# Performance work log

Measured on AMD Instinct MI355X. Metric: run time of the kernel, lower is better.

The kernel has to match this reference:

```python
import jax, jax.numpy as jnp
import numpy as np

BN_EPS = 1e-5
K = 3  # number of nearest neighbors for interpolation


def setup_inputs() -> dict:
    key = jax.random.key(0)
    ks = jax.random.split(key, 16)
    B, N1, N2 = 8, 8192, 2048
    C2, C1, H = 256, 128, 256  # in_channels, skip_channels, out_channels
    total_in = C2 + C1
    inp = {
        "xyz1": jax.random.normal(ks[0], (B, 3, N1), dtype=jnp.float32),
        "xyz2": jax.random.normal(ks[1], (B, 3, N2), dtype=jnp.float32),
        "features1": jax.random.normal(ks[2], (B, C1, N1), dtype=jnp.float32),
        "features2": jax.random.normal(ks[3], (B, C2, N2), dtype=jnp.float32),
        # SharedMLP([total_in, H, H]): two 1x1 Conv1d + BatchNorm1d (eval mode) + ReLU
        "w1": jax.random.normal(ks[4], (H, total_in), dtype=jnp.float32) * 0.05,
        "b1": jax.random.normal(ks[5], (H,), dtype=jnp.float32) * 0.01,
        "g1": 1.0 + 0.1 * jax.random.normal(ks[6], (H,), dtype=jnp.float32),
        "be1": 0.1 * jax.random.normal(ks[7], (H,), dtype=jnp.float32),
        "m1": 0.1 * jax.random.normal(ks[8], (H,), dtype=jnp.float32),
        "v1": 0.5 + jax.random.uniform(ks[9], (H,), dtype=jnp.float32),
        "w2": jax.random.normal(ks[10], (H, H), dtype=jnp.float32) * 0.05,
        "b2": jax.random.normal(ks[11], (H,), dtype=jnp.float32) * 0.01,
        "g2": 1.0 + 0.1 * jax.random.normal(ks[12], (H,), dtype=jnp.float32),
        "be2": 0.1 * jax.random.normal(ks[13], (H,), dtype=jnp.float32),
        "m2": 0.1 * jax.random.normal(ks[14], (H,), dtype=jnp.float32),
        "v2": 0.5 + jax.random.uniform(ks[15], (H,), dtype=jnp.float32),
    }
    return inp


def _conv_bn_relu(x, w, b, g, be, m, v):
    # x: [B, Cin, N], w: [Cout, Cin] (1x1 conv), BN in eval mode
    y = jnp.einsum("oc,bcn->bon", w, x) + b[None, :, None]
    y = (y - m[None, :, None]) * (g / jnp.sqrt(v + BN_EPS))[None, :, None] + be[None, :, None]
    return jax.nn.relu(y)


def reference(xyz1, xyz2, features1, features2,
              w1, b1, g1, be1, m1, v1,
              w2, b2, g2, be2, m2, v2):
    # --- squared pairwise distances [B, N1, N2] ---
    x1 = jnp.transpose(xyz1, (0, 2, 1))  # [B, N1, 3]
    x2 = jnp.transpose(xyz2, (0, 2, 1))  # [B, N2, 3]
    sq = (jnp.sum(x1 * x1, axis=-1, keepdims=True)
          + jnp.sum(x2 * x2, axis=-1)[:, None, :]
          - 2.0 * jnp.einsum("bnd,bmd->bnm", x1, x2))
    # --- k=3 nearest neighbors (smallest sq distances) ---
    neg_d, idx = jax.lax.top_k(-sq, K)          # [B, N1, K]
    dist = jnp.maximum(-neg_d, 1e-10)
    weight = 1.0 / dist
    weight = weight / jnp.sum(weight, axis=-1, keepdims=True)  # [B, N1, K]
    # --- gather neighbor features and inverse-distance interpolate ---
    feat2_t = jnp.transpose(features2, (0, 2, 1))              # [B, N2, C2]
    neighbor = jax.vmap(lambda f, i: f[i])(feat2_t, idx)       # [B, N1, K, C2]
    interp = jnp.einsum("bnkc,bnk->bnc", neighbor, weight)     # [B, N1, C2]
    interp = jnp.transpose(interp, (0, 2, 1))                  # [B, C2, N1]
    # --- concat skip features and shared MLP ---
    x = jnp.concatenate([interp, features1], axis=1)           # [B, C2+C1, N1]
    x = _conv_bn_relu(x, w1, b1, g1, be1, m1, v1)
    x = _conv_bn_relu(x, w2, b2, g2, be2, m2, v2)
    return x
```

## Files before the change

kernel.cpp:

```cpp
#include <hip/hip_runtime.h>
#include <hip/hip_bf16.h>

typedef unsigned short u16;
typedef __attribute__((ext_vector_type(4))) float f32x4;
typedef __attribute__((ext_vector_type(8))) short short8;

#define BN_EPS 1e-5f

__device__ __forceinline__ u16 f2b(float x) {
  union { float f; unsigned int u; } v; v.f = x;
  unsigned int r = (v.u + 0x7FFFu + ((v.u >> 16) & 1u)) >> 16;
  return (u16)r;
}
__device__ __forceinline__ float b2f(u16 u) {
  union { unsigned int u; float f; } v; v.u = ((unsigned int)u) << 16;
  return v.f;
}
__device__ __forceinline__ float asf(unsigned u) {
  union { unsigned u; float f; } v; v.u = u; return v.f;
}

__global__ void prep_transpose_kernel(
    const float* __restrict__ f2, u16* __restrict__ f2t,
    const float* __restrict__ w1, const float* __restrict__ b1,
    const float* __restrict__ g1, const float* __restrict__ be1,
    const float* __restrict__ m1, const float* __restrict__ v1,
    const float* __restrict__ w2, const float* __restrict__ b2,
    const float* __restrict__ g2, const float* __restrict__ be2,
    const float* __restrict__ m2, const float* __restrict__ v2,
    u16* __restrict__ w1b, u16* __restrict__ w2b,
    float* __restrict__ al1, float* __restrict__ bt1,
    float* __restrict__ al2, float* __restrict__ bt2) {
  __shared__ float tile[32][33];
  int t = threadIdx.x;
  int blk = blockIdx.x;
  if (blk < 4096) {
    int tx = t & 31, ty = t >> 5;
    int b = (blk >> 9) & 7;
    int n2t = (blk & 63) * 32, ct = ((blk >> 6) & 7) * 32;
#pragma unroll
    for (int i = 0; i < 4; ++i) {
      int c = ct + ty + i * 8;
      tile[ty + i * 8][tx] = f2[((size_t)b * 256 + c) * 2048 + n2t + tx];
    }
    __syncthreads();
#pragma unroll
    for (int i = 0; i < 4; ++i) {
      int n2 = n2t + ty + i * 8;
      f2t[((size_t)b * 2048 + n2) * 256 + ct + tx] = f2b(tile[tx][ty + i * 8]);
    }
  } else if (blk < 4480) {
    int id = (blk - 4096) * 256 + t;
    unsigned o = (unsigned)id / 384u;
    unsigned c = (unsigned)id % 384u;
    w1b[(c >> 5) * 8192 + o * 32 + (c & 31)] = f2b(w1[id]);
  } else if (blk < 4736) {
    int j = (blk - 4480) * 256 + t;
    unsigned o = (unsigned)j >> 8;
    unsigned c = (unsigned)j & 255u;
    w2b[(c >> 5) * 8192 + o * 32 + (c & 31)] = f2b(w2[j]);
  } else if (blk == 4736) {
    float a = g1[t] / sqrtf(v1[t] + BN_EPS);
    al1[t] = a;
    bt1[t] = (b1[t] - m1[t]) * a + be1[t];
  } else {
    float a = g2[t] / sqrtf(v2[t] + BN_EPS);
    al2[t] = a;
    bt2[t] = (b2[t] - m2[t]) * a + be2[t];
  }
}

__global__ __launch_bounds__(256) void knn_interp_kernel(
    const float* __restrict__ xyz1, const float* __restrict__ xyz2,
    const float* __restrict__ f1, const u16* __restrict__ f2t,
    u16* __restrict__ xb) {
  union Lds {
    struct { float4 pts[2048]; float md[256 * 3]; u16 mi[256 * 3]; } a;
    float f1t[128 * 65];
  };
  __shared__ Lds lds;
  __shared__ float wts[64 * 3];
  __shared__ int idxs[64 * 3];

  int t = threadIdx.x;
  int b = blockIdx.x >> 7;
  int n1_0 = (blockIdx.x & 127) * 64;
  int panel = blockIdx.x;

  const float* x2 = xyz2 + b * 3 * 2048;
  for (int j = t; j < 2048; j += 256) {
    float cx = x2[j], cy = x2[2048 + j], cz = x2[4096 + j];
    float nsq = (cx * cx + cy * cy) + cz * cz;
    lds.a.pts[j] = make_float4(cx, cy, cz, nsq);
  }
  __syncthreads();

  const float* x1 = xyz1 + b * 3 * 8192;

  {
    int p = t & 63, s = t >> 6;
    int n1 = n1_0 + p;
    float bx = x1[n1], by = x1[8192 + n1], bz = x1[16384 + n1];
    float nx = -2.f * bx, ny = -2.f * by, nz = -2.f * bz;
    float d0 = 3.4e38f, d1 = 3.4e38f, d2 = 3.4e38f;
    int i0 = 0, i1 = 0, i2 = 0;
    int jb = s * 512;

#define KNN_UPD(cv, jv)                                                      \
    {                                                                        \
      float sq = fmaf(nx, (cv).x, fmaf(ny, (cv).y, fmaf(nz, (cv).z, (cv).w))); \
      if (__any(sq < d2)) {                                                  \
        bool c0 = sq < d0, c1 = sq < d1, c2 = sq < d2;                       \
        i2 = c1 ? i1 : (c2 ? (jv) : i2);                                     \
        i1 = c0 ? i0 : (c1 ? (jv) : i1);                                     \
        i0 = c0 ? (jv) : i0;                                                 \
        d2 = __builtin_amdgcn_fmed3f(sq, d1, d2);                            \
        d1 = __builtin_amdgcn_fmed3f(sq, d0, d1);                            \
        d0 = fminf(sq, d0);                                                  \
      }                                                                      \
    }

    for (int jj = 0; jj < 512; jj += 4) {
      float4 ca = lds.a.pts[jb + jj + 0];
      float4 cb = lds.a.pts[jb + jj + 1];
      float4 cc = lds.a.pts[jb + jj + 2];
      float4 cd = lds.a.pts[jb + jj + 3];
      KNN_UPD(ca, jb + jj + 0);
      KNN_UPD(cb, jb + jj + 1);
      KNN_UPD(cc, jb + jj + 2);
      KNN_UPD(cd, jb + jj + 3);
    }
#undef KNN_UPD
    lds.a.md[t * 3 + 0] = d0; lds.a.md[t * 3 + 1] = d1; lds.a.md[t * 3 + 2] = d2;
    lds.a.mi[t * 3 + 0] = (u16)i0; lds.a.mi[t * 3 + 1] = (u16)i1; lds.a.mi[t * 3 + 2] = (u16)i2;
  }
  __syncthreads();
  if (t < 64) {
    float d0 = 3.4e38f, d1 = 3.4e38f, d2 = 3.4e38f;
    int i0 = 0, i1 = 0, i2 = 0;
#pragma unroll
    for (int s = 0; s < 4; ++s) {
#pragma unroll
      for (int k = 0; k < 3; ++k) {
        float d = lds.a.md[(s * 64 + t) * 3 + k];
        int i = (int)lds.a.mi[(s * 64 + t) * 3 + k];
        bool c0 = d < d0, c1 = d < d1, c2 = d < d2;
        i2 = c1 ? i1 : (c2 ? i : i2);
        i1 = c0 ? i0 : (c1 ? i : i1);
        i0 = c0 ? i : i0;
        d2 = c1 ? d1 : (c2 ? d : d2);
        d1 = c0 ? d0 : (c1 ? d : d1);
        d0 = c0 ? d : d0;
      }
    }
    int n1 = n1_0 + t;
    float bx = x1[n1], by = x1[8192 + n1], bz = x1[16384 + n1];
    float nn = (bx * bx + by * by) + bz * bz;
    float e0 = fmaxf(d0 + nn, 1e-10f), e1 = fmaxf(d1 + nn, 1e-10f), e2 = fmaxf(d2 + nn, 1e-10f);
    float w0 = 1.0f / e0, w1 = 1.0f / e1, w2 = 1.0f / e2;
    float sm = (w0 + w1) + w2;
    wts[t * 3 + 0] = w0 / sm; wts[t * 3 + 1] = w1 / sm; wts[t * 3 + 2] = w2 / sm;
    idxs[t * 3 + 0] = i0 * 256; idxs[t * 3 + 1] = i1 * 256; idxs[t * 3 + 2] = i2 * 256;
  }
  __syncthreads();

  {
    const u16* f2tb = f2t + (size_t)b * 2048 * 256;
    int tc = t & 63;
    int qg = t >> 6;
    int ce = (4 * tc) & 31;
    size_t xbase = (size_t)panel * 24576 + (size_t)(tc >> 3) * 2048 + ce;
#pragma unroll 4
    for (int p2 = 0; p2 < 16; ++p2) {
      int p = p2 * 4 + qg;
      int j0 = idxs[p * 3 + 0], j1 = idxs[p * 3 + 1], j2 = idxs[p * 3 + 2];
      float w0 = wts[p * 3 + 0], w1 = wts[p * 3 + 1], w2 = wts[p * 3 + 2];
      uint2 a0 = *(const uint2*)&f2tb[j0 + 4 * tc];
      uint2 a1 = *(const uint2*)&f2tb[j1 + 4 * tc];
      uint2 a2 = *(const uint2*)&f2tb[j2 + 4 * tc];
      float v0 = (w0 * asf(a0.x << 16) + w1 * asf(a1.x << 16)) + w2 * asf(a2.x << 16);
      float v1 = (w0 * asf(a0.x & 0xffff0000u) + w1 * asf(a1.x & 0xffff0000u))
                 + w2 * asf(a2.x & 0xffff0000u);
      float v2 = (w0 * asf(a0.y << 16) + w1 * asf(a1.y << 16)) + w2 * asf(a2.y << 16);
      float v3 = (w0 * asf(a0.y & 0xffff0000u) + w1 * asf(a1.y & 0xffff0000u))
                 + w2 * asf(a2.y & 0xffff0000u);
      uint2 pk;
      pk.x = (unsigned)f2b(v0) | ((unsigned)f2b(v1) << 16);
      pk.y = (unsigned)f2b(v2) | ((unsigned)f2b(v3) << 16);
      *(uint2*)&xb[xbase + (size_t)p * 32] = pk;
    }
  }
  __syncthreads();

  {
    const float* f1b = f1 + (size_t)b * 128 * 8192 + n1_0;
    for (int it = 0; it < 32; ++it) {
      int c = it * 4 + (t >> 6);
      int n = t & 63;
      lds.f1t[c * 65 + n] = f1b[(size_t)c * 8192 + n];
    }
    __syncthreads();
    for (int it = 0; it < 32; ++it) {
      int v = it * 256 + t;
      int c = v & 127, p = v >> 7;
      float val = lds.f1t[c * 65 + p];
      xb[(size_t)panel * 24576 + (size_t)(8 + (c >> 5)) * 2048 + p * 32 + (c & 31)] = f2b(val);
    }
  }
}

__global__ __launch_bounds__(256) void gemm_fused_kernel(
    const u16* __restrict__ xin, const u16* __restrict__ w1b,
    const u16* __restrict__ w2b,
    const float* __restrict__ al1, const float* __restrict__ bt1,
    const float* __restrict__ al2, const float* __restrict__ bt2,
    float* __restrict__ fout) {
  __shared__ u16 y1t[8 * 64 * 40];
  int t = threadIdx.x;
  int panel = blockIdx.x;
  int w = t >> 6, lane = t & 63, l15 = lane & 15, quad = lane >> 4;

  f32x4 acc[4][4];
#pragma unroll
  for (int m = 0; m < 4; ++m)
#pragma unroll
    for (int n = 0; n < 4; ++n)
      acc[m][n] = (f32x4){0.f, 0.f, 0.f, 0.f};

  {
    const u16* aw = w1b + (size_t)(w * 64 + l15) * 32 + quad * 8;
    const u16* bx = xin + (size_t)panel * 24576 + (size_t)l15 * 32 + quad * 8;
    short8 af[2][4], bf[2][4];
#pragma unroll
    for (int m = 0; m < 4; ++m)
      af[0][m] = *(const short8*)(aw + m * 512);
#pragma unroll
    for (int n = 0; n < 4; ++n)
      bf[0][n] = *(const short8*)(bx + n * 512);
#pragma unroll
    for (int kt = 0; kt < 12; ++kt) {
      int cur = kt & 1, nxt = cur ^ 1;
      if (kt < 11) {
#pragma unroll
        for (int m = 0; m < 4; ++m)
          af[nxt][m] = *(const short8*)(aw + (kt + 1) * 8192 + m * 512);
#pragma unroll
        for (int n = 0; n < 4; ++n)
          bf[nxt][n] = *(const short8*)(bx + (kt + 1) * 2048 + n * 512);
      }
#pragma unroll
      for (int m = 0; m < 4; ++m)
#pragma unroll
        for (int n = 0; n < 4; ++n)
          acc[m][n] = __builtin_amdgcn_mfma_f32_16x16x32_bf16(af[cur][m], bf[cur][n], acc[m][n], 0, 0, 0);
    }
  }

  {
    float al[4][4], bt[4][4];
#pragma unroll
    for (int m = 0; m < 4; ++m)
#pragma unroll
      for (int r = 0; r < 4; ++r) {
        int o = w * 64 + m * 16 + quad * 4 + r;
        al[m][r] = al1[o];
        bt[m][r] = bt1[o];
      }
#pragma unroll
    for (int m = 0; m < 4; ++m) {
      int kt2 = w * 2 + (m >> 1);
      int osub = (m & 1) * 16 + quad * 4;
#pragma unroll
      for (int n = 0; n < 4; ++n) {
        int col = n * 16 + l15;
        ushort4 pk;
        pk.x = f2b(fmaxf(fmaf(al[m][0], acc[m][n][0], bt[m][0]), 0.f));
        pk.y = f2b(fmaxf(fmaf(al[m][1], acc[m][n][1], bt[m][1]), 0.f));
        pk.z = f2b(fmaxf(fmaf(al[m][2], acc[m][n][2], bt[m][2]), 0.f));
        pk.w = f2b(fmaxf(fmaf(al[m][3], acc[m][n][3], bt[m][3]), 0.f));
        *(ushort4*)&y1t[(kt2 * 64 + col) * 40 + osub] = pk;
      }
    }
  }
  __syncthreads();

#pragma unroll
  for (int m = 0; m < 4; ++m)
#pragma unroll
    for (int n = 0; n < 4; ++n)
      acc[m][n] = (f32x4){0.f, 0.f, 0.f, 0.f};
  {
    const u16* aw = w2b + (size_t)(w * 64 + l15) * 32 + quad * 8;
    short8 af[2][4];
#pragma unroll
    for (int m = 0; m < 4; ++m)
      af[0][m] = *(const short8*)(aw + m * 512);
#pragma unroll
    for (int kt = 0; kt < 8; ++kt) {
      int cur = kt & 1, nxt = cur ^ 1;
      if (kt < 7) {
#pragma unroll
        for (int m = 0; m < 4; ++m)
          af[nxt][m] = *(const short8*)(aw + (kt + 1) * 8192 + m * 512);
      }
      short8 bf[4];
#pragma unroll
      for (int n = 0; n < 4; ++n)
        bf[n] = *(const short8*)&y1t[(kt * 64 + n * 16 + l15) * 40 + quad * 8];
#pragma unroll
      for (int m = 0; m < 4; ++m)
#pragma unroll
        for (int n = 0; n < 4; ++n)
          acc[m][n] = __builtin_amdgcn_mfma_f32_16x16x32_bf16(af[cur][m], bf[n], acc[m][n], 0, 0, 0);
    }
  }

  {
    float al[4][4], bt[4][4];
#pragma unroll
    for (int m = 0; m < 4; ++m)
#pragma unroll
      for (int r = 0; r < 4; ++r) {
        int o = w * 64 + m * 16 + quad * 4 + r;
        al[m][r] = al2[o];
        bt[m][r] = bt2[o];
      }
    int bb = panel >> 7;
    int n1base = (panel & 127) * 64;
#pragma unroll
    for (int m = 0; m < 4; ++m)
#pragma unroll
      for (int n = 0; n < 4; ++n) {
        int col = n * 16 + l15;
#pragma unroll
        for (int r = 0; r < 4; ++r) {
          int o = w * 64 + m * 16 + quad * 4 + r;
          float vv = fmaxf(fmaf(al[m][r], acc[m][n][r], bt[m][r]), 0.f);
          fout[(size_t)(bb * 256 + o) * 8192 + n1base + col] = vv;
        }
      }
  }
}

extern "C" void kernel_launch(void* const* d_in, const int* in_sizes, int n_in,
                              void* d_out, int out_size, void* d_ws, size_t ws_size,
                              hipStream_t stream) {
  const float* xyz1 = (const float*)d_in[0];
  const float* xyz2 = (const float*)d_in[1];
  const float* f1   = (const float*)d_in[2];
  const float* f2   = (const float*)d_in[3];
  const float* w1   = (const float*)d_in[4];
  const float* b1   = (const float*)d_in[5];
  const float* g1   = (const float*)d_in[6];
  const float* be1  = (const float*)d_in[7];
  const float* m1   = (const float*)d_in[8];
  const float* v1   = (const float*)d_in[9];
  const float* w2   = (const float*)d_in[10];
  const float* b2   = (const float*)d_in[11];
  const float* g2   = (const float*)d_in[12];
  const float* be2  = (const float*)d_in[13];
  const float* m2   = (const float*)d_in[14];
  const float* v2   = (const float*)d_in[15];

  char* ws = (char*)d_ws;
  u16* xb   = (u16*)(ws);
  u16* f2t  = (u16*)(ws + 50331648);
  u16* w1b  = (u16*)(ws + 83886080);
  u16* w2b  = (u16*)(ws + 84082688);
  float* al1 = (float*)(ws + 84213760);
  float* bt1 = (float*)(ws + 84214784);
  float* al2 = (float*)(ws + 84215808);
  float* bt2 = (float*)(ws + 84216832);
  float* out = (float*)d_out;

  prep_transpose_kernel<<<4738, 256, 0, stream>>>(
      f2, f2t, w1, b1, g1, be1, m1, v1, w2, b2, g2, be2, m2, v2,
      w1b, w2b, al1, bt1, al2, bt2);
  knn_interp_kernel<<<1024, 256, 0, stream>>>(xyz1, xyz2, f1, f2t, xb);
  gemm_fused_kernel<<<1024, 256, 0, stream>>>(xb, w1b, w2b, al1, bt1, al2, bt2, out);
}
```

Before: 217.4 us.

## Precompute xyz2 float4 table in prep kernel and read KNN candidates from global

Moves the per-block packing of xyz2 into (x,y,z,|x|^2) float4 entries out of the KNN kernel and into extra blocks of the prep kernel, which write a global table. The KNN loop then reads candidate points straight from global memory (uniform addresses, so effectively scalar or broadcast loads through cache) instead of staging 32KB in LDS. This removes the LDS fill, a barrier and most of the LDS footprint, which can raise occupancy. The cost is that the inner loop now depends on global or cache load latency instead of LDS reads.

```diff
diff --git a/kernel.cpp b/kernel.cpp
--- a/kernel.cpp
+++ b/kernel.cpp
@@ -28,9 +28,11 @@
     const float* __restrict__ w2, const float* __restrict__ b2,
     const float* __restrict__ g2, const float* __restrict__ be2,
     const float* __restrict__ m2, const float* __restrict__ v2,
+    const float* __restrict__ xyz2,
     u16* __restrict__ w1b, u16* __restrict__ w2b,
     float* __restrict__ al1, float* __restrict__ bt1,
-    float* __restrict__ al2, float* __restrict__ bt2) {
+    float* __restrict__ al2, float* __restrict__ bt2,
+    float4* __restrict__ c4i) {
   __shared__ float tile[32][33];
   int t = threadIdx.x;
   int blk = blockIdx.x;
@@ -63,19 +65,27 @@
     float a = g1[t] / sqrtf(v1[t] + BN_EPS);
     al1[t] = a;
     bt1[t] = (b1[t] - m1[t]) * a + be1[t];
-  } else {
+  } else if (blk == 4737) {
     float a = g2[t] / sqrtf(v2[t] + BN_EPS);
     al2[t] = a;
     bt2[t] = (b2[t] - m2[t]) * a + be2[t];
+  } else {
+    int idx = (blk - 4738) * 256 + t;
+    int bb = idx >> 11, j = idx & 2047;
+    float cx = xyz2[bb * 6144 + j];
+    float cy = xyz2[bb * 6144 + 2048 + j];
+    float cz = xyz2[bb * 6144 + 4096 + j];
+    float nsq = (cx * cx + cy * cy) + cz * cz;
+    c4i[bb * 2048 + j] = make_float4(cx, cy, cz, nsq);
   }
 }
 
 __global__ __launch_bounds__(256) void knn_interp_kernel(
-    const float* __restrict__ xyz1, const float* __restrict__ xyz2,
+    const float* __restrict__ xyz1, const float4* __restrict__ c4i,
     const float* __restrict__ f1, const u16* __restrict__ f2t,
     u16* __restrict__ xb) {
   union Lds {
-    struct { float4 pts[2048]; float md[256 * 3]; u16 mi[256 * 3]; } a;
+    struct { float md[256 * 3]; u16 mi[256 * 3]; } a;
     float f1t[128 * 65];
   };
   __shared__ Lds lds;
@@ -87,14 +97,6 @@
   int n1_0 = (blockIdx.x & 127) * 64;
   int panel = blockIdx.x;
 
-  const float* x2 = xyz2 + b * 3 * 2048;
-  for (int j = t; j < 2048; j += 256) {
-    float cx = x2[j], cy = x2[2048 + j], cz = x2[4096 + j];
-    float nsq = (cx * cx + cy * cy) + cz * cz;
-    lds.a.pts[j] = make_float4(cx, cy, cz, nsq);
-  }
-  __syncthreads();
-
   const float* x1 = xyz1 + b * 3 * 8192;
 
   {
@@ -102,6 +104,7 @@
     int n1 = n1_0 + p;
     float bx = x1[n1], by = x1[8192 + n1], bz = x1[16384 + n1];
     float nx = -2.f * bx, ny = -2.f * by, nz = -2.f * bz;
+    const float4* cp = c4i + b * 2048;
     float d0 = 3.4e38f, d1 = 3.4e38f, d2 = 3.4e38f;
     int i0 = 0, i1 = 0, i2 = 0;
     int jb = s * 512;
@@ -121,10 +124,10 @@
     }
 
     for (int jj = 0; jj < 512; jj += 4) {
-      float4 ca = lds.a.pts[jb + jj + 0];
-      float4 cb = lds.a.pts[jb + jj + 1];
-      float4 cc = lds.a.pts[jb + jj + 2];
-      float4 cd = lds.a.pts[jb + jj + 3];
+      float4 ca = cp[jb + jj + 0];
+      float4 cb = cp[jb + jj + 1];
+      float4 cc = cp[jb + jj + 2];
+      float4 cd = cp[jb + jj + 3];
       KNN_UPD(ca, jb + jj + 0);
       KNN_UPD(cb, jb + jj + 1);
       KNN_UPD(cc, jb + jj + 2);
@@ -363,19 +366,20 @@
   const float* v2   = (const float*)d_in[15];
 
   char* ws = (char*)d_ws;
-  u16* xb   = (u16*)(ws);
-  u16* f2t  = (u16*)(ws + 50331648);
-  u16* w1b  = (u16*)(ws + 83886080);
-  u16* w2b  = (u16*)(ws + 84082688);
+  u16* xb    = (u16*)(ws);
+  u16* f2t   = (u16*)(ws + 50331648);
+  float4* c4i = (float4*)(ws + 58720256);
+  u16* w1b   = (u16*)(ws + 83886080);
+  u16* w2b   = (u16*)(ws + 84082688);
   float* al1 = (float*)(ws + 84213760);
   float* bt1 = (float*)(ws + 84214784);
   float* al2 = (float*)(ws + 84215808);
   float* bt2 = (float*)(ws + 84216832);
   float* out = (float*)d_out;
 
-  prep_transpose_kernel<<<4738, 256, 0, stream>>>(
+  prep_transpose_kernel<<<4802, 256, 0, stream>>>(
       f2, f2t, w1, b1, g1, be1, m1, v1, w2, b2, g2, be2, m2, v2,
-      w1b, w2b, al1, bt1, al2, bt2);
-  knn_interp_kernel<<<1024, 256, 0, stream>>>(xyz1, xyz2, f1, f2t, xb);
+      xyz2, w1b, w2b, al1, bt1, al2, bt2, c4i);
+  knn_interp_kernel<<<1024, 256, 0, stream>>>(xyz1, c4i, f1, f2t, xb);
   gemm_fused_kernel<<<1024, 256, 0, stream>>>(xb, w1b, w2b, al1, bt1, al2, bt2, out);
 }
```

Result: slower. 240.8 us (+10.8%).

## Fuse kNN interpolation and MLP GEMMs into one kernel via LDS staging

Applied to the files above, without the earlier changes.

Merges the kNN/interpolation kernel and the two-layer MLP GEMM kernel into a single kernel per 64-point panel. The concatenated bf16 input tile is built directly in shared memory (Bt) rather than written to a global workspace and read back. This removes a global round trip of the activation buffer and one kernel launch. In exchange, shared-memory use per block grows, which may reduce occupancy, and the kNN phase and the MFMA phase can no longer overlap across separate kernels.

```diff
diff --git a/kernel.cpp b/kernel.cpp
--- a/kernel.cpp
+++ b/kernel.cpp
@@ -70,28 +70,33 @@
   }
 }
 
-__global__ __launch_bounds__(256) void knn_interp_kernel(
+__global__ __launch_bounds__(256) void fp_fused_kernel(
     const float* __restrict__ xyz1, const float* __restrict__ xyz2,
     const float* __restrict__ f1, const u16* __restrict__ f2t,
-    u16* __restrict__ xb) {
-  union Lds {
+    const u16* __restrict__ w1b, const u16* __restrict__ w2b,
+    const float* __restrict__ al1, const float* __restrict__ bt1,
+    const float* __restrict__ al2, const float* __restrict__ bt2,
+    float* __restrict__ fout) {
+  union U {
     struct { float4 pts[2048]; float md[256 * 3]; u16 mi[256 * 3]; } a;
     float f1t[128 * 65];
+    u16 y1t[8 * 64 * 40];
   };
-  __shared__ Lds lds;
+  __shared__ U u;
+  __shared__ u16 Bt[12 * 64 * 40];
   __shared__ float wts[64 * 3];
   __shared__ int idxs[64 * 3];
 
   int t = threadIdx.x;
-  int b = blockIdx.x >> 7;
-  int n1_0 = (blockIdx.x & 127) * 64;
   int panel = blockIdx.x;
+  int b = panel >> 7;
+  int n1_0 = (panel & 127) * 64;
 
   const float* x2 = xyz2 + b * 3 * 2048;
   for (int j = t; j < 2048; j += 256) {
     float cx = x2[j], cy = x2[2048 + j], cz = x2[4096 + j];
     float nsq = (cx * cx + cy * cy) + cz * cz;
-    lds.a.pts[j] = make_float4(cx, cy, cz, nsq);
+    u.a.pts[j] = make_float4(cx, cy, cz, nsq);
   }
   __syncthreads();
 
@@ -121,18 +126,18 @@
     }
 
     for (int jj = 0; jj < 512; jj += 4) {
-      float4 ca = lds.a.pts[jb + jj + 0];
-      float4 cb = lds.a.pts[jb + jj + 1];
-      float4 cc = lds.a.pts[jb + jj + 2];
-      float4 cd = lds.a.pts[jb + jj + 3];
+      float4 ca = u.a.pts[jb + jj + 0];
+      float4 cb = u.a.pts[jb + jj + 1];
+      float4 cc = u.a.pts[jb + jj + 2];
+      float4 cd = u.a.pts[jb + jj + 3];
       KNN_UPD(ca, jb + jj + 0);
       KNN_UPD(cb, jb + jj + 1);
       KNN_UPD(cc, jb + jj + 2);
       KNN_UPD(cd, jb + jj + 3);
     }
 #undef KNN_UPD
-    lds.a.md[t * 3 + 0] = d0; lds.a.md[t * 3 + 1] = d1; lds.a.md[t * 3 + 2] = d2;
-    lds.a.mi[t * 3 + 0] = (u16)i0; lds.a.mi[t * 3 + 1] = (u16)i1; lds.a.mi[t * 3 + 2] = (u16)i2;
+    u.a.md[t * 3 + 0] = d0; u.a.md[t * 3 + 1] = d1; u.a.md[t * 3 + 2] = d2;
+    u.a.mi[t * 3 + 0] = (u16)i0; u.a.mi[t * 3 + 1] = (u16)i1; u.a.mi[t * 3 + 2] = (u16)i2;
   }
   __syncthreads();
   if (t < 64) {
@@ -142,8 +147,8 @@
     for (int s = 0; s < 4; ++s) {
 #pragma unroll
       for (int k = 0; k < 3; ++k) {
-        float d = lds.a.md[(s * 64 + t) * 3 + k];
-        int i = (int)lds.a.mi[(s * 64 + t) * 3 + k];
+        float d = u.a.md[(s * 64 + t) * 3 + k];
+        int i = (int)u.a.mi[(s * 64 + t) * 3 + k];
         bool c0 = d < d0, c1 = d < d1, c2 = d < d2;
         i2 = c1 ? i1 : (c2 ? i : i2);
         i1 = c0 ? i0 : (c1 ? i : i1);
@@ -169,7 +174,7 @@
     int tc = t & 63;
     int qg = t >> 6;
     int ce = (4 * tc) & 31;
-    size_t xbase = (size_t)panel * 24576 + (size_t)(tc >> 3) * 2048 + ce;
+    int bbase = (tc >> 3) * 2560 + ce;
 #pragma unroll 4
     for (int p2 = 0; p2 < 16; ++p2) {
       int p = p2 * 4 + qg;
@@ -187,37 +192,27 @@
       uint2 pk;
       pk.x = (unsigned)f2b(v0) | ((unsigned)f2b(v1) << 16);
       pk.y = (unsigned)f2b(v2) | ((unsigned)f2b(v3) << 16);
-      *(uint2*)&xb[xbase + (size_t)p * 32] = pk;
-    }
-  }
-  __syncthreads();
+      *(uint2*)&Bt[bbase + p * 40] = pk;
+    }
+  }
 
   {
     const float* f1b = f1 + (size_t)b * 128 * 8192 + n1_0;
     for (int it = 0; it < 32; ++it) {
       int c = it * 4 + (t >> 6);
       int n = t & 63;
-      lds.f1t[c * 65 + n] = f1b[(size_t)c * 8192 + n];
+      u.f1t[c * 65 + n] = f1b[(size_t)c * 8192 + n];
     }
     __syncthreads();
     for (int it = 0; it < 32; ++it) {
       int v = it * 256 + t;
       int c = v & 127, p = v >> 7;
-      float val = lds.f1t[c * 65 + p];
-      xb[(size_t)panel * 24576 + (size_t)(8 + (c >> 5)) * 2048 + p * 32 + (c & 31)] = f2b(val);
-    }
-  }
-}
-
-__global__ __launch_bounds__(256) void gemm_fused_kernel(
-    const u16* __restrict__ xin, const u16* __restrict__ w1b,
-    const u16* __restrict__ w2b,
-    const float* __restrict__ al1, const float* __restrict__ bt1,
-    const float* __restrict__ al2, const float* __restrict__ bt2,
-    float* __restrict__ fout) {
-  __shared__ u16 y1t[8 * 64 * 40];
-  int t = threadIdx.x;
-  int panel = blockIdx.x;
+      float val = u.f1t[c * 65 + p];
+      Bt[(8 + (c >> 5)) * 2560 + p * 40 + (c & 31)] = f2b(val);
+    }
+  }
+  __syncthreads();
+
   int w = t >> 6, lane = t & 63, l15 = lane & 15, quad = lane >> 4;
 
   f32x4 acc[4][4];
@@ -229,14 +224,10 @@
 
   {
     const u16* aw = w1b + (size_t)(w * 64 + l15) * 32 + quad * 8;
-    const u16* bx = xin + (size_t)panel * 24576 + (size_t)l15 * 32 + quad * 8;
-    short8 af[2][4], bf[2][4];
+    short8 af[2][4];
 #pragma unroll
     for (int m = 0; m < 4; ++m)
       af[0][m] = *(const short8*)(aw + m * 512);
-#pragma unroll
-    for (int n = 0; n < 4; ++n)
-      bf[0][n] = *(const short8*)(bx + n * 512);
 #pragma unroll
     for (int kt = 0; kt < 12; ++kt) {
       int cur = kt & 1, nxt = cur ^ 1;
@@ -244,15 +235,16 @@
 #pragma unroll
         for (int m = 0; m < 4; ++m)
           af[nxt][m] = *(const short8*)(aw + (kt + 1) * 8192 + m * 512);
+      }
+      short8 bf[4];
+#pragma unroll
+      for (int n = 0; n < 4; ++n)
+        bf[n] = *(const short8*)&Bt[kt * 2560 + (n * 16 + l15) * 40 + quad * 8];
+#pragma unroll
+      for (int m = 0; m < 4; ++m)
 #pragma unroll
         for (int n = 0; n < 4; ++n)
-          bf[nxt][n] = *(const short8*)(bx + (kt + 1) * 2048 + n * 512);
-      }
-#pragma unroll
-      for (int m = 0; m < 4; ++m)
-#pragma unroll
-        for (int n = 0; n < 4; ++n)
-          acc[m][n] = __builtin_amdgcn_mfma_f32_16x16x32_bf16(af[cur][m], bf[cur][n], acc[m][n], 0, 0, 0);
+          acc[m][n] = __builtin_amdgcn_mfma_f32_16x16x32_bf16(af[cur][m], bf[n], acc[m][n], 0, 0, 0);
     }
   }
 
@@ -278,7 +270,7 @@
         pk.y = f2b(fmaxf(fmaf(al[m][1], acc[m][n][1], bt[m][1]), 0.f));
         pk.z = f2b(fmaxf(fmaf(al[m][2], acc[m][n][2], bt[m][2]), 0.f));
         pk.w = f2b(fmaxf(fmaf(al[m][3], acc[m][n][3], bt[m][3]), 0.f));
-        *(ushort4*)&y1t[(kt2 * 64 + col) * 40 + osub] = pk;
+        *(ushort4*)&u.y1t[(kt2 * 64 + col) * 40 + osub] = pk;
       }
     }
   }
@@ -306,7 +298,7 @@
       short8 bf[4];
 #pragma unroll
       for (int n = 0; n < 4; ++n)
-        bf[n] = *(const short8*)&y1t[(kt * 64 + n * 16 + l15) * 40 + quad * 8];
+        bf[n] = *(const short8*)&u.y1t[(kt * 64 + n * 16 + l15) * 40 + quad * 8];
 #pragma unroll
       for (int m = 0; m < 4; ++m)
 #pragma unroll
@@ -325,8 +317,6 @@
         al[m][r] = al2[o];
         bt[m][r] = bt2[o];
       }
-    int bb = panel >> 7;
-    int n1base = (panel & 127) * 64;
 #pragma unroll
     for (int m = 0; m < 4; ++m)
 #pragma unroll
@@ -336,7 +326,7 @@
         for (int r = 0; r < 4; ++r) {
           int o = w * 64 + m * 16 + quad * 4 + r;
           float vv = fmaxf(fmaf(al[m][r], acc[m][n][r], bt[m][r]), 0.f);
-          fout[(size_t)(bb * 256 + o) * 8192 + n1base + col] = vv;
+          fout[(size_t)(b * 256 + o) * 8192 + n1_0 + col] = vv;
         }
       }
   }
@@ -363,10 +353,9 @@
   const float* v2   = (const float*)d_in[15];
 
   char* ws = (char*)d_ws;
-  u16* xb   = (u16*)(ws);
-  u16* f2t  = (u16*)(ws + 50331648);
-  u16* w1b  = (u16*)(ws + 83886080);
-  u16* w2b  = (u16*)(ws + 84082688);
+  u16* f2t   = (u16*)(ws + 50331648);
+  u16* w1b   = (u16*)(ws + 83886080);
+  u16* w2b   = (u16*)(ws + 84082688);
   float* al1 = (float*)(ws + 84213760);
   float* bt1 = (float*)(ws + 84214784);
   float* al2 = (float*)(ws + 84215808);
@@ -376,6 +365,6 @@
   prep_transpose_kernel<<<4738, 256, 0, stream>>>(
       f2, f2t, w1, b1, g1, be1, m1, v1, w2, b2, g2, be2, m2, v2,
       w1b, w2b, al1, bt1, al2, bt2);
-  knn_interp_kernel<<<1024, 256, 0, stream>>>(xyz1, xyz2, f1, f2t, xb);
-  gemm_fused_kernel<<<1024, 256, 0, stream>>>(xb, w1b, w2b, al1, bt1, al2, bt2, out);
-}
+  fp_fused_kernel<<<1024, 256, 0, stream>>>(
+      xyz1, xyz2, f1, f2t, w1b, w2b, al1, bt1, al2, bt2, out);
+}
```

After: 316.1 us. +45.4%, slower.

## Process two query points per thread in KNN kernel to amortize LDS reads

Applied to the files above, without the earlier changes.

Each KNN block now handles 128 query points instead of 64, with every thread tracking top-3 for two queries against the same candidate loaded from LDS. This halves the number of blocks and the repeated loading of xyz2 into LDS, and doubles the arithmetic done per LDS read. The interpolation and feature-transpose phases are reorganised to cover two output panels per block. In exchange the grid shrinks to 512 blocks on a 256-CU device, the wave-wide branch is taken whenever either query improves, and register pressure goes up.

```diff
diff --git a/kernel.cpp b/kernel.cpp
--- a/kernel.cpp
+++ b/kernel.cpp
@@ -75,17 +75,19 @@
     const float* __restrict__ f1, const u16* __restrict__ f2t,
     u16* __restrict__ xb) {
   union Lds {
-    struct { float4 pts[2048]; float md[256 * 3]; u16 mi[256 * 3]; } a;
-    float f1t[128 * 65];
+    struct { float4 pts[2048]; float md[256 * 6]; u16 mi[256 * 6]; } a;
+    float f1t[64 * 129];
   };
   __shared__ Lds lds;
-  __shared__ float wts[64 * 3];
-  __shared__ int idxs[64 * 3];
+  __shared__ float wts[128 * 3];
+  __shared__ int idxs[128 * 3];
 
   int t = threadIdx.x;
-  int b = blockIdx.x >> 7;
-  int n1_0 = (blockIdx.x & 127) * 64;
-  int panel = blockIdx.x;
+  int blk = blockIdx.x;
+  int b = blk >> 6;
+  int tp = blk & 63;
+  int n1_0 = tp * 128;
+  int p0 = b * 128 + tp * 2;
 
   const float* x2 = xyz2 + b * 3 * 2048;
   for (int j = t; j < 2048; j += 256) {
@@ -99,24 +101,36 @@
 
   {
     int p = t & 63, s = t >> 6;
-    int n1 = n1_0 + p;
-    float bx = x1[n1], by = x1[8192 + n1], bz = x1[16384 + n1];
-    float nx = -2.f * bx, ny = -2.f * by, nz = -2.f * bz;
-    float d0 = 3.4e38f, d1 = 3.4e38f, d2 = 3.4e38f;
-    int i0 = 0, i1 = 0, i2 = 0;
+    int na = n1_0 + p;
+    int nb = n1_0 + 64 + p;
+    float axq = x1[na], ayq = x1[8192 + na], azq = x1[16384 + na];
+    float bxq = x1[nb], byq = x1[8192 + nb], bzq = x1[16384 + nb];
+    float nxa = -2.f * axq, nya = -2.f * ayq, nza = -2.f * azq;
+    float nxb = -2.f * bxq, nyb = -2.f * byq, nzb = -2.f * bzq;
+    float da0 = 3.4e38f, da1 = 3.4e38f, da2 = 3.4e38f;
+    float db0 = 3.4e38f, db1 = 3.4e38f, db2 = 3.4e38f;
+    int ia0 = 0, ia1 = 0, ia2 = 0, ib0 = 0, ib1 = 0, ib2 = 0;
     int jb = s * 512;
 
-#define KNN_UPD(cv, jv)                                                      \
+#define KNN_UPD2(cv, jv)                                                     \
     {                                                                        \
-      float sq = fmaf(nx, (cv).x, fmaf(ny, (cv).y, fmaf(nz, (cv).z, (cv).w))); \
-      if (__any(sq < d2)) {                                                  \
-        bool c0 = sq < d0, c1 = sq < d1, c2 = sq < d2;                       \
-        i2 = c1 ? i1 : (c2 ? (jv) : i2);                                     \
-        i1 = c0 ? i0 : (c1 ? (jv) : i1);                                     \
-        i0 = c0 ? (jv) : i0;                                                 \
-        d2 = __builtin_amdgcn_fmed3f(sq, d1, d2);                            \
-        d1 = __builtin_amdgcn_fmed3f(sq, d0, d1);                            \
-        d0 = fminf(sq, d0);                                                  \
+      float sqa = fmaf(nxa, (cv).x, fmaf(nya, (cv).y, fmaf(nza, (cv).z, (cv).w))); \
+      float sqb = fmaf(nxb, (cv).x, fmaf(nyb, (cv).y, fmaf(nzb, (cv).z, (cv).w))); \
+      if (__any((sqa < da2) || (sqb < db2))) {                               \
+        bool a0 = sqa < da0, a1 = sqa < da1, a2 = sqa < da2;                 \
+        ia2 = a1 ? ia1 : (a2 ? (jv) : ia2);                                  \
+        ia1 = a0 ? ia0 : (a1 ? (jv) : ia1);                                  \
+        ia0 = a0 ? (jv) : ia0;                                               \
+        da2 = __builtin_amdgcn_fmed3f(sqa, da1, da2);                        \
+        da1 = __builtin_amdgcn_fmed3f(sqa, da0, da1);                        \
+        da0 = fminf(sqa, da0);                                               \
+        bool b0 = sqb < db0, b1 = sqb < db1, b2 = sqb < db2;                 \
+        ib2 = b1 ? ib1 : (b2 ? (jv) : ib2);                                  \
+        ib1 = b0 ? ib0 : (b1 ? (jv) : ib1);                                  \
+        ib0 = b0 ? (jv) : ib0;                                               \
+        db2 = __builtin_amdgcn_fmed3f(sqb, db1, db2);                        \
+        db1 = __builtin_amdgcn_fmed3f(sqb, db0, db1);                        \
+        db0 = fminf(sqb, db0);                                               \
       }                                                                      \
     }
 
@@ -125,25 +139,28 @@
       float4 cb = lds.a.pts[jb + jj + 1];
       float4 cc = lds.a.pts[jb + jj + 2];
       float4 cd = lds.a.pts[jb + jj + 3];
-      KNN_UPD(ca, jb + jj + 0);
-      KNN_UPD(cb, jb + jj + 1);
-      KNN_UPD(cc, jb + jj + 2);
-      KNN_UPD(cd, jb + jj + 3);
-    }
-#undef KNN_UPD
-    lds.a.md[t * 3 + 0] = d0; lds.a.md[t * 3 + 1] = d1; lds.a.md[t * 3 + 2] = d2;
-    lds.a.mi[t * 3 + 0] = (u16)i0; lds.a.mi[t * 3 + 1] = (u16)i1; lds.a.mi[t * 3 + 2] = (u16)i2;
+      KNN_UPD2(ca, jb + jj + 0);
+      KNN_UPD2(cb, jb + jj + 1);
+      KNN_UPD2(cc, jb + jj + 2);
+      KNN_UPD2(cd, jb + jj + 3);
+    }
+#undef KNN_UPD2
+    lds.a.md[t * 6 + 0] = da0; lds.a.md[t * 6 + 1] = da1; lds.a.md[t * 6 + 2] = da2;
+    lds.a.md[t * 6 + 3] = db0; lds.a.md[t * 6 + 4] = db1; lds.a.md[t * 6 + 5] = db2;
+    lds.a.mi[t * 6 + 0] = (u16)ia0; lds.a.mi[t * 6 + 1] = (u16)ia1; lds.a.mi[t * 6 + 2] = (u16)ia2;
+    lds.a.mi[t * 6 + 3] = (u16)ib0; lds.a.mi[t * 6 + 4] = (u16)ib1; lds.a.mi[t * 6 + 5] = (u16)ib2;
   }
   __syncthreads();
-  if (t < 64) {
+  if (t < 128) {
+    int p = t & 63, side = t >> 6;
     float d0 = 3.4e38f, d1 = 3.4e38f, d2 = 3.4e38f;
     int i0 = 0, i1 = 0, i2 = 0;
 #pragma unroll
     for (int s = 0; s < 4; ++s) {
 #pragma unroll
       for (int k = 0; k < 3; ++k) {
-        float d = lds.a.md[(s * 64 + t) * 3 + k];
-        int i = (int)lds.a.mi[(s * 64 + t) * 3 + k];
+        float d = lds.a.md[(s * 64 + p) * 6 + side * 3 + k];
+        int i = (int)lds.a.mi[(s * 64 + p) * 6 + side * 3 + k];
         bool c0 = d < d0, c1 = d < d1, c2 = d < d2;
         i2 = c1 ? i1 : (c2 ? i : i2);
         i1 = c0 ? i0 : (c1 ? i : i1);
@@ -169,9 +186,9 @@
     int tc = t & 63;
     int qg = t >> 6;
     int ce = (4 * tc) & 31;
-    size_t xbase = (size_t)panel * 24576 + (size_t)(tc >> 3) * 2048 + ce;
+    int ktoff = (tc >> 3) * 2048 + ce;
 #pragma unroll 4
-    for (int p2 = 0; p2 < 16; ++p2) {
+    for (int p2 = 0; p2 < 32; ++p2) {
       int p = p2 * 4 + qg;
       int j0 = idxs[p * 3 + 0], j1 = idxs[p * 3 + 1], j2 = idxs[p * 3 + 2];
       float w0 = wts[p * 3 + 0], w1 = wts[p * 3 + 1], w2 = wts[p * 3 + 2];
@@ -187,24 +204,32 @@
       uint2 pk;
       pk.x = (unsigned)f2b(v0) | ((unsigned)f2b(v1) << 16);
       pk.y = (unsigned)f2b(v2) | ((unsigned)f2b(v3) << 16);
-      *(uint2*)&xb[xbase + (size_t)p * 32] = pk;
-    }
-  }
-  __syncthreads();
+      size_t xaddr = (size_t)(p0 + (p >> 6)) * 24576 + ktoff + (size_t)(p & 63) * 32;
+      *(uint2*)&xb[xaddr] = pk;
+    }
+  }
 
   {
     const float* f1b = f1 + (size_t)b * 128 * 8192 + n1_0;
-    for (int it = 0; it < 32; ++it) {
-      int c = it * 4 + (t >> 6);
-      int n = t & 63;
-      lds.f1t[c * 65 + n] = f1b[(size_t)c * 8192 + n];
-    }
-    __syncthreads();
-    for (int it = 0; it < 32; ++it) {
-      int v = it * 256 + t;
-      int c = v & 127, p = v >> 7;
-      float val = lds.f1t[c * 65 + p];
-      xb[(size_t)panel * 24576 + (size_t)(8 + (c >> 5)) * 2048 + p * 32 + (c & 31)] = f2b(val);
+#pragma unroll
+    for (int h = 0; h < 2; ++h) {
+      __syncthreads();
+      for (int it = 0; it < 32; ++it) {
+        int c = it * 2 + (t >> 7);
+        int n = t & 127;
+        lds.f1t[c * 129 + n] = f1b[(size_t)(h * 64 + c) * 8192 + n];
+      }
+      __syncthreads();
+      for (int it = 0; it < 32; ++it) {
+        int v = it * 256 + t;
+        int c = v & 63, p = v >> 6;
+        int ch = h * 64 + c;
+        float val = lds.f1t[c * 129 + p];
+        size_t xaddr = (size_t)(p0 + (p >> 6)) * 24576
+                     + (size_t)(8 + (ch >> 5)) * 2048
+                     + (size_t)(p & 63) * 32 + (ch & 31);
+        xb[xaddr] = f2b(val);
+      }
     }
   }
 }
@@ -376,6 +401,6 @@
   prep_transpose_kernel<<<4738, 256, 0, stream>>>(
       f2, f2t, w1, b1, g1, be1, m1, v1, w2, b2, g2, be2, m2, v2,
       w1b, w2b, al1, bt1, al2, bt2);
-  knn_interp_kernel<<<1024, 256, 0, stream>>>(xyz1, xyz2, f1, f2t, xb);
+  knn_interp_kernel<<<512, 256, 0, stream>>>(xyz1, xyz2, f1, f2t, xb);
   gemm_fused_kernel<<<1024, 256, 0, stream>>>(xb, w1b, w2b, al1, bt1, al2, bt2, out);
 }
```

Result: slower. 242.7 us (+11.6%).
